# Optimization experiments

Hardware: AMD Instinct MI355X
Metric: run time of the kernel (lower is better)

## Reference

```python
import jax, jax.numpy as jnp
import numpy as np
from jax import lax

N = 50000        # num nodes
E = 800000       # edges per relation (no self loops; N self loops appended)
R = 3            # num_relations
F_IN = 256       # feature_size
C = 128          # hid_dim / channels
B = 4096         # batch_nodes
DT = 0.25
NSTEPS = 4       # n = ceil(time/dt) = ceil(1.0/0.25)


def setup_inputs() -> dict:
    key = jax.random.key(0)
    k1, k2, k3, k4, k5, k6, k7, k8 = jax.random.split(key, 8)
    features = jax.random.normal(k1, (N, F_IN), dtype=jnp.float32)
    # edges with no self loops: dst = (src + off) mod N, off in [1, N)
    src = jax.random.randint(k2, (R, E), 0, N)
    off = jax.random.randint(k3, (R, E), 1, N)
    dst = (src + off) % N
    edge_index = jnp.stack([src, dst], axis=1).astype(jnp.int64)  # [R, 2, E]
    batch_nodes = jax.random.randint(k4, (B,), 0, N).astype(jnp.int64)
    s = 1.0 / np.sqrt(F_IN)
    lin0_w = jax.random.normal(k5, (R, C, F_IN), dtype=jnp.float32) * s
    lin0_b = jax.random.normal(k6, (R, C), dtype=jnp.float32) * 0.01
    lin1_w = jax.random.normal(k7, (R, C, F_IN), dtype=jnp.float32) * s
    lin1_b = jax.random.normal(k8, (R, C), dtype=jnp.float32) * 0.01
    return {"features": features, "edge_index": edge_index, "batch_nodes": batch_nodes,
            "lin0_w": lin0_w, "lin0_b": lin0_b, "lin1_w": lin1_w, "lin1_b": lin1_b}


def _propagate(x, row, col, w):
    # out[i] = sum_{e: col[e]==i} w[e] * x[row[e]]   (gather-scale-scatter SpMM)
    return jax.ops.segment_sum(w[:, None] * x[row], col, num_segments=N)


def _wave_pde(x, row, col, w0, b0, w1, b1):
    # add_remaining_self_loops(fill=0.0): self loops appended at end with weight 0
    loops = jnp.arange(N, dtype=row.dtype)
    row_f = jnp.concatenate([row, loops])
    col_f = jnp.concatenate([col, loops])
    w_f = jnp.concatenate([jnp.ones((E,), x.dtype), jnp.zeros((N,), x.dtype)])
    # sym normalization: D^-1/2 A D^-1/2 (deg over col)
    deg = jax.ops.segment_sum(w_f, col_f, num_segments=N)
    dinv = jnp.where(deg > 0, lax.rsqrt(jnp.maximum(deg, 1e-30)), 0.0)
    w_norm = dinv[row_f] * w_f * dinv[col_f]
    # set_init_value
    phi0 = x @ w0.T + b0
    phi1 = x @ w1.T + b1
    # exp_conv_0 (exp_init=True): w' = dt^2*w/2; diag += 1; x1 = dt*phi1 + prop(phi0)
    w_init = (DT * DT * 0.5) * w_norm
    w_init = w_init.at[E:].add(1.0)
    x1 = DT * phi1 + _propagate(phi0, row_f, col_f, w_init)
    # time-stepping convs: w'' = dt^2*w; diag += 2; x_next = prop(x) - x_pre
    w_step = (DT * DT) * w_norm
    w_step = w_step.at[E:].add(2.0)

    def step(carry, _):
        xc, xp = carry
        xn = _propagate(xc, row_f, col_f, w_step) - xp
        return (xn, xc), None

    (x_out, _), _ = lax.scan(step, (x1, phi0), None, length=NSTEPS - 1)
    return x_out


def reference(features, edge_index, batch_nodes, lin0_w, lin0_b, lin1_w, lin1_b):
    # eval mode: dropout is identity
    embeds = []
    for r in range(R):
        row = edge_index[r, 0]
        col = edge_index[r, 1]
        x = _wave_pde(features, row, col, lin0_w[r], lin0_b[r], lin1_w[r], lin1_b[r])
        embeds.append(x[batch_nodes])  # [B, C]
    multi = jnp.stack(embeds, axis=1)  # [B, R, C]
    return multi.reshape(B, R * C)
```

## Files before the change

kernel.cpp:

```cpp
#include <hip/hip_runtime.h>
#include <hip/hip_bf16.h>

#define N_NODES 50000
#define N_EDGES 800000
#define N_REL   3
#define F_IN    256
#define CH      128
#define BATCH   4096
#define DT      0.25f

typedef __bf16 bf16x8 __attribute__((ext_vector_type(8)));
typedef float f32x4 __attribute__((ext_vector_type(4)));

__device__ __forceinline__ ushort f2bf(float f) {
  unsigned u = __float_as_uint(f);
  return (ushort)((u + 0x7FFFu + ((u >> 16) & 1u)) >> 16);
}
__device__ __forceinline__ float bf2f(ushort h) {
  return __uint_as_float((unsigned)h << 16);
}

__global__ void k_detect(const int* __restrict__ ei, int* __restrict__ flag) {
  int lane = threadIdx.x;
  int v = ei[2 * lane + 1];
  unsigned long long m = __ballot(v != 0);
  if (lane == 0) flag[0] = (m == 0ull) ? 1 : 0;
}

__global__ void k_hist3(const int* __restrict__ ei, const int* __restrict__ flag,
                        int* __restrict__ deg3) {
  int e = blockIdx.x * 256 + threadIdx.x;
  int r = blockIdx.y;
  if (e >= N_EDGES) return;
  long ci = (long)r * 2 * N_EDGES + N_EDGES + e;
  int d = flag[0] ? ei[2 * ci] : ei[ci];
  atomicAdd(&deg3[r * N_NODES + d], 1);
}

__global__ void k_dinv3(const int* __restrict__ deg3, float* __restrict__ dinv3) {
  int i = blockIdx.x * blockDim.x + threadIdx.x;
  if (i >= 3 * N_NODES) return;
  int d = deg3[i];
  dinv3[i] = d > 0 ? rsqrtf((float)d) : 0.0f;
}

__global__ void k_scan3(const int* __restrict__ deg3, int* __restrict__ off3) {
  __shared__ int sm[1024];
  const int* deg = deg3 + blockIdx.x * N_NODES;
  int* off = off3 + blockIdx.x * (N_NODES + 1);
  int tid = threadIdx.x;
  const int PER = (N_NODES + 1023) / 1024;
  int base = tid * PER;
  int s = 0;
  for (int i = 0; i < PER; ++i) { int idx = base + i; if (idx < N_NODES) s += deg[idx]; }
  sm[tid] = s;
  __syncthreads();
  for (int d = 1; d < 1024; d <<= 1) {
    int v = 0;
    if (tid >= d) v = sm[tid - d];
    __syncthreads();
    sm[tid] += v;
    __syncthreads();
  }
  int run = sm[tid] - s;
  for (int i = 0; i < PER; ++i) {
    int idx = base + i;
    if (idx < N_NODES) { off[idx] = run; run += deg[idx]; }
  }
  if (tid == 1023) off[N_NODES] = run;
}

__global__ void k_fill3(const int* __restrict__ ei, const int* __restrict__ flag,
                        const int* __restrict__ off3, int* __restrict__ cur3,
                        const float* __restrict__ dinv3, int2* __restrict__ csr) {
  int e = blockIdx.x * 256 + threadIdx.x;
  int r = blockIdx.y;
  if (e >= N_EDGES) return;
  int i64 = flag[0];
  long ri = (long)r * 2 * N_EDGES + e;
  long ci = ri + N_EDGES;
  int s = i64 ? ei[2 * ri] : ei[ri];
  int d = i64 ? ei[2 * ci] : ei[ci];
  const float* dinv = dinv3 + r * N_NODES;
  int pos = atomicAdd(&cur3[r * N_NODES + d], 1);
  int slot = off3[r * (N_NODES + 1) + d] + pos;
  csr[(size_t)r * N_EDGES + slot] = make_int2(s, __float_as_int(dinv[s] * dinv[d]));
}

__global__ __launch_bounds__(256) void k_phi_mfma(
    const float* __restrict__ X, const float* __restrict__ W0,
    const float* __restrict__ b0, const float* __restrict__ W1,
    const float* __restrict__ b1, float* __restrict__ P0,
    float* __restrict__ P1) {
  __shared__ ushort Ah[128 * 32], Al[128 * 32], Bh[128 * 32], Bl[128 * 32];
  const int tid = threadIdx.x;
  const int m0 = blockIdx.x * 128;
  const float* W = blockIdx.y ? W1 : W0;
  const float* bias = blockIdx.y ? b1 : b0;
  float* P = blockIdx.y ? P1 : P0;
  const int wid = tid >> 6, lane = tid & 63;
  const int wr = wid >> 1, wc = wid & 1;
  const int lr = lane & 15, k8 = lane >> 4;
  const int rt = tid >> 1, kb = (tid & 1) * 16;
  const bool mok = (m0 + rt) < N_NODES;
  const float* Xrow = X + (size_t)(m0 + rt) * F_IN;
  const float* Wrow = W + (size_t)rt * F_IN;
  f32x4 acc[4][4] = {};
  for (int k0 = 0; k0 < F_IN; k0 += 32) {
    float4 xa[4], wb[4];
#pragma unroll
    for (int j = 0; j < 4; ++j) {
      xa[j] = mok ? *(const float4*)(Xrow + k0 + kb + 4 * j)
                  : make_float4(0.f, 0.f, 0.f, 0.f);
      wb[j] = *(const float4*)(Wrow + k0 + kb + 4 * j);
    }
    if (k0) __syncthreads();
#pragma unroll
    for (int j = 0; j < 4; ++j) {
      int idx = rt * 32 + kb + 4 * j;
      ushort h0 = f2bf(xa[j].x), h1 = f2bf(xa[j].y), h2 = f2bf(xa[j].z), h3 = f2bf(xa[j].w);
      *(ushort4*)&Ah[idx] = make_ushort4(h0, h1, h2, h3);
      *(ushort4*)&Al[idx] =
          make_ushort4(f2bf(xa[j].x - bf2f(h0)), f2bf(xa[j].y - bf2f(h1)),
                       f2bf(xa[j].z - bf2f(h2)), f2bf(xa[j].w - bf2f(h3)));
      ushort g0 = f2bf(wb[j].x), g1 = f2bf(wb[j].y), g2 = f2bf(wb[j].z), g3 = f2bf(wb[j].w);
      *(ushort4*)&Bh[idx] = make_ushort4(g0, g1, g2, g3);
      *(ushort4*)&Bl[idx] =
          make_ushort4(f2bf(wb[j].x - bf2f(g0)), f2bf(wb[j].y - bf2f(g1)),
                       f2bf(wb[j].z - bf2f(g2)), f2bf(wb[j].w - bf2f(g3)));
    }
    __syncthreads();
    bf16x8 ah[4], al[4], bh[4], bl[4];
#pragma unroll
    for (int i = 0; i < 4; ++i) {
      int ao = (wr * 64 + i * 16 + lr) * 32 + k8 * 8;
      int bo = (wc * 64 + i * 16 + lr) * 32 + k8 * 8;
      ah[i] = *(const bf16x8*)&Ah[ao];
      al[i] = *(const bf16x8*)&Al[ao];
      bh[i] = *(const bf16x8*)&Bh[bo];
      bl[i] = *(const bf16x8*)&Bl[bo];
    }
#pragma unroll
    for (int i = 0; i < 4; ++i)
#pragma unroll
      for (int j = 0; j < 4; ++j) {
        acc[i][j] = __builtin_amdgcn_mfma_f32_16x16x32_bf16(ah[i], bh[j], acc[i][j], 0, 0, 0);
        acc[i][j] = __builtin_amdgcn_mfma_f32_16x16x32_bf16(ah[i], bl[j], acc[i][j], 0, 0, 0);
        acc[i][j] = __builtin_amdgcn_mfma_f32_16x16x32_bf16(al[i], bh[j], acc[i][j], 0, 0, 0);
      }
  }
#pragma unroll
  for (int j = 0; j < 4; ++j) {
    int ch = wc * 64 + j * 16 + lr;
    float bv = bias[ch];
#pragma unroll
    for (int i = 0; i < 4; ++i) {
      int mbase = m0 + wr * 64 + i * 16 + k8 * 4;
#pragma unroll
      for (int q = 0; q < 4; ++q) {
        int m = mbase + q;
        if (m < N_NODES) P[(size_t)m * CH + ch] = acc[i][j][q] + bv;
      }
    }
  }
}

__global__ __launch_bounds__(256, 6) void k_prop(
    const float* __restrict__ xc, const float* __restrict__ other,
    float* __restrict__ out, const int* __restrict__ off,
    const int2* __restrict__ csr, float wscale, float aself, float beta) {
  int node = blockIdx.x * 4 + (threadIdx.x >> 6);
  if (node >= N_NODES) return;
  int lane = threadIdx.x & 63;
  int g = lane >> 4, l = lane & 15;
  int e0 = off[node], e1 = off[node + 1];
  size_t base = (size_t)node * CH;
  int go = (g & 1) * 64;
  float4 sv = *(const float4*)(xc + base + go + 4 * l);
  float4 ov = *(const float4*)(other + base + go + 4 * l);
  float4 acc0 = make_float4(0.f, 0.f, 0.f, 0.f);
  float4 acc1 = make_float4(0.f, 0.f, 0.f, 0.f);
  for (int e = e0; e < e1; e += 16) {
    int lim = e1 - 1;
    int2 pm[4];
    float wgt[4];
#pragma unroll
    for (int u = 0; u < 4; ++u) {
      int ee = e + 4 * u + g;
      pm[u] = csr[min(ee, lim)];
      wgt[u] = (ee <= lim) ? __int_as_float(pm[u].y) : 0.f;
    }
    float4 va[4], vb[4];
#pragma unroll
    for (int u = 0; u < 4; ++u) {
      const float4* rs = (const float4*)(xc + (size_t)pm[u].x * CH);
      va[u] = rs[l];
      vb[u] = rs[l + 16];
    }
#pragma unroll
    for (int u = 0; u < 4; ++u) {
      float w0 = wgt[u];
      acc0.x = fmaf(w0, va[u].x, acc0.x); acc0.y = fmaf(w0, va[u].y, acc0.y);
      acc0.z = fmaf(w0, va[u].z, acc0.z); acc0.w = fmaf(w0, va[u].w, acc0.w);
      acc1.x = fmaf(w0, vb[u].x, acc1.x); acc1.y = fmaf(w0, vb[u].y, acc1.y);
      acc1.z = fmaf(w0, vb[u].z, acc1.z); acc1.w = fmaf(w0, vb[u].w, acc1.w);
    }
  }
#pragma unroll
  for (int m = 16; m < 64; m <<= 1) {
    acc0.x += __shfl_xor(acc0.x, m); acc0.y += __shfl_xor(acc0.y, m);
    acc0.z += __shfl_xor(acc0.z, m); acc0.w += __shfl_xor(acc0.w, m);
    acc1.x += __shfl_xor(acc1.x, m); acc1.y += __shfl_xor(acc1.y, m);
    acc1.z += __shfl_xor(acc1.z, m); acc1.w += __shfl_xor(acc1.w, m);
  }
  if (g == 0) {
    float4 o;
    o.x = wscale * acc0.x + aself * sv.x + beta * ov.x;
    o.y = wscale * acc0.y + aself * sv.y + beta * ov.y;
    o.z = wscale * acc0.z + aself * sv.z + beta * ov.z;
    o.w = wscale * acc0.w + aself * sv.w + beta * ov.w;
    *(float4*)(out + base + 4 * l) = o;
  } else if (g == 1) {
    float4 o;
    o.x = wscale * acc1.x + aself * sv.x + beta * ov.x;
    o.y = wscale * acc1.y + aself * sv.y + beta * ov.y;
    o.z = wscale * acc1.z + aself * sv.z + beta * ov.z;
    o.w = wscale * acc1.w + aself * sv.w + beta * ov.w;
    *(float4*)(out + base + 64 + 4 * l) = o;
  }
}

__global__ void k_gather(const float* __restrict__ x, const int* __restrict__ batch,
                         const int* __restrict__ flag, float* __restrict__ out, int r) {
  int idx = blockIdx.x * blockDim.x + threadIdx.x;
  int b = idx >> 6, lane = idx & 63;
  if (b >= BATCH) return;
  int i64 = flag[0];
  int node = i64 ? batch[2 * b] : batch[b];
  ((float2*)out)[(size_t)b * (N_REL * 64) + r * 64 + lane] =
      ((const float2*)x)[(size_t)node * 64 + lane];
}

extern "C" void kernel_launch(void* const* d_in, const int* in_sizes, int n_in,
                              void* d_out, int out_size, void* d_ws, size_t ws_size,
                              hipStream_t stream) {
  const float* features   = (const float*)d_in[0];
  const int*   edge_index = (const int*)d_in[1];
  const int*   batch_nodes= (const int*)d_in[2];
  const float* lin0_w     = (const float*)d_in[3];
  const float* lin0_b     = (const float*)d_in[4];
  const float* lin1_w     = (const float*)d_in[5];
  const float* lin1_b     = (const float*)d_in[6];
  float* out = (float*)d_out;

  char* w = (char*)d_ws;
  size_t o = 0;
  auto nxt = [&](size_t bytes) {
    char* p = w + o;
    o = (o + bytes + 255) & ~(size_t)255;
    return p;
  };
  int*   flag  = (int*)  nxt(256);
  int*   deg3  = (int*)  nxt((size_t)3 * N_NODES * 4);
  int*   cur3  = (int*)  nxt((size_t)3 * N_NODES * 4);
  float* dinv3 = (float*)nxt((size_t)3 * N_NODES * 4);
  int*   off3  = (int*)  nxt((size_t)3 * (N_NODES + 1) * 4);
  int2*  csr   = (int2*) nxt((size_t)3 * N_EDGES * 8);
  float* P0    = (float*)nxt((size_t)N_NODES * CH * 4);
  float* P1    = (float*)nxt((size_t)N_NODES * CH * 4);
  float* Ab    = (float*)nxt((size_t)N_NODES * CH * 4);

  k_detect<<<1, 64, 0, stream>>>(edge_index, flag);
  hipMemsetAsync(deg3, 0, (size_t)3 * N_NODES * 4, stream);
  hipMemsetAsync(cur3, 0, (size_t)3 * N_NODES * 4, stream);
  k_hist3<<<dim3((N_EDGES + 255) / 256, 3), 256, 0, stream>>>(edge_index, flag, deg3);
  k_dinv3<<<(3 * N_NODES + 255) / 256, 256, 0, stream>>>(deg3, dinv3);
  k_scan3<<<3, 1024, 0, stream>>>(deg3, off3);
  k_fill3<<<dim3((N_EDGES + 255) / 256, 3), 256, 0, stream>>>(edge_index, flag, off3,
                                                              cur3, dinv3, csr);

  const float h2 = DT * DT;
  for (int r = 0; r < N_REL; ++r) {
    const int*  offr = off3 + r * (N_NODES + 1);
    const int2* csrr = csr + (size_t)r * N_EDGES;
    k_phi_mfma<<<dim3((N_NODES + 127) / 128, 2), 256, 0, stream>>>(
        features, lin0_w + (size_t)r * CH * F_IN, lin0_b + (size_t)r * CH,
        lin1_w + (size_t)r * CH * F_IN, lin1_b + (size_t)r * CH, P0, P1);
    k_prop<<<(N_NODES + 3) / 4, 256, 0, stream>>>(P0, P1, Ab, offr, csrr,
                                                  0.5f * h2, 1.0f, DT);
    k_prop<<<(N_NODES + 3) / 4, 256, 0, stream>>>(Ab, P0, P0, offr, csrr,
                                                  h2, 2.0f, -1.0f);
    k_prop<<<(N_NODES + 3) / 4, 256, 0, stream>>>(P0, Ab, Ab, offr, csrr,
                                                  h2, 2.0f, -1.0f);
    k_prop<<<(N_NODES + 3) / 4, 256, 0, stream>>>(Ab, P0, P0, offr, csrr,
                                                  h2, 2.0f, -1.0f);
    k_gather<<<(BATCH * 64 + 255) / 256, 256, 0, stream>>>(P0, batch_nodes, flag, out, r);
  }
}
```

Measured before the change: 1.323 ms.

## Rescale features by D^-1/2, drop edge weights, fuse last propagation with batch gather

When every node has nonzero degree, the symmetric normalisation is folded into the features: phi outputs are pre-scaled by dinv, the CSR holds only source indices (halving edge traffic), and each propagation divides by the node degree, with a sqrt(deg) rescale at the output. A device flag set when any node has zero degree keeps the old weighted path as a fallback. The final time step is computed only for the batch nodes and written straight to the output, skipping one full-graph propagation per relation and the separate gather kernel. The change adds a branch on a runtime flag inside the hot loop and alters the floating-point rounding order.

```diff
diff --git a/kernel.cpp b/kernel.cpp
--- a/kernel.cpp
+++ b/kernel.cpp
@@ -37,11 +37,17 @@
   atomicAdd(&deg3[r * N_NODES + d], 1);
 }
 
-__global__ void k_dinv3(const int* __restrict__ deg3, float* __restrict__ dinv3) {
+__global__ void k_dinv3(const int* __restrict__ deg3, float* __restrict__ dinv3,
+                        int* __restrict__ flag) {
   int i = blockIdx.x * blockDim.x + threadIdx.x;
   if (i >= 3 * N_NODES) return;
   int d = deg3[i];
-  dinv3[i] = d > 0 ? rsqrtf((float)d) : 0.0f;
+  if (d > 0) {
+    dinv3[i] = rsqrtf((float)d);
+  } else {
+    dinv3[i] = 0.0f;
+    atomicOr(&flag[1], 1);
+  }
 }
 
 __global__ void k_scan3(const int* __restrict__ deg3, int* __restrict__ off3) {
@@ -72,25 +78,31 @@
 
 __global__ void k_fill3(const int* __restrict__ ei, const int* __restrict__ flag,
                         const int* __restrict__ off3, int* __restrict__ cur3,
-                        const float* __restrict__ dinv3, int2* __restrict__ csr) {
+                        const float* __restrict__ dinv3, void* __restrict__ csrv) {
   int e = blockIdx.x * 256 + threadIdx.x;
   int r = blockIdx.y;
   if (e >= N_EDGES) return;
-  int i64 = flag[0];
+  int i64 = flag[0], iso = flag[1];
   long ri = (long)r * 2 * N_EDGES + e;
   long ci = ri + N_EDGES;
   int s = i64 ? ei[2 * ri] : ei[ri];
   int d = i64 ? ei[2 * ci] : ei[ci];
-  const float* dinv = dinv3 + r * N_NODES;
   int pos = atomicAdd(&cur3[r * N_NODES + d], 1);
   int slot = off3[r * (N_NODES + 1) + d] + pos;
-  csr[(size_t)r * N_EDGES + slot] = make_int2(s, __float_as_int(dinv[s] * dinv[d]));
+  if (iso) {
+    const float* dinv = dinv3 + r * N_NODES;
+    ((int2*)csrv)[(size_t)r * N_EDGES + slot] =
+        make_int2(s, __float_as_int(dinv[s] * dinv[d]));
+  } else {
+    ((int*)csrv)[(size_t)r * N_EDGES + slot] = s;
+  }
 }
 
 __global__ __launch_bounds__(256) void k_phi_mfma(
     const float* __restrict__ X, const float* __restrict__ W0,
     const float* __restrict__ b0, const float* __restrict__ W1,
-    const float* __restrict__ b1, float* __restrict__ P0,
+    const float* __restrict__ b1, const float* __restrict__ dinv,
+    const int* __restrict__ flag, float* __restrict__ P0,
     float* __restrict__ P1) {
   __shared__ ushort Ah[128 * 32], Al[128 * 32], Bh[128 * 32], Bl[128 * 32];
   const int tid = threadIdx.x;
@@ -149,6 +161,15 @@
         acc[i][j] = __builtin_amdgcn_mfma_f32_16x16x32_bf16(al[i], bh[j], acc[i][j], 0, 0, 0);
       }
   }
+  int iso = flag[1];
+  float rsc[4][4];
+#pragma unroll
+  for (int i = 0; i < 4; ++i)
+#pragma unroll
+    for (int q = 0; q < 4; ++q) {
+      int m = m0 + wr * 64 + i * 16 + k8 * 4 + q;
+      rsc[i][q] = (m < N_NODES && !iso) ? dinv[m] : 1.0f;
+    }
 #pragma unroll
   for (int j = 0; j < 4; ++j) {
     int ch = wc * 64 + j * 16 + lr;
@@ -159,7 +180,67 @@
 #pragma unroll
       for (int q = 0; q < 4; ++q) {
         int m = mbase + q;
-        if (m < N_NODES) P[(size_t)m * CH + ch] = acc[i][j][q] + bv;
+        if (m < N_NODES) P[(size_t)m * CH + ch] = (acc[i][j][q] + bv) * rsc[i][q];
+      }
+    }
+  }
+}
+
+__device__ __forceinline__ void prop_accum(
+    const float* __restrict__ xc, const void* __restrict__ csrv, int r, int iso,
+    int e0, int e1, int g, int l, float4& acc0, float4& acc1) {
+  if (!iso) {
+    const int* csr = (const int*)csrv + (size_t)r * N_EDGES;
+    for (int e = e0; e < e1; e += 16) {
+      int lim = e1 - 1;
+      int src[4]; float wgt[4];
+#pragma unroll
+      for (int u = 0; u < 4; ++u) {
+        int ee = e + 4 * u + g;
+        src[u] = csr[min(ee, lim)];
+        wgt[u] = (ee <= lim) ? 1.f : 0.f;
+      }
+      float4 va[4], vb[4];
+#pragma unroll
+      for (int u = 0; u < 4; ++u) {
+        const float4* rs = (const float4*)(xc + (size_t)src[u] * CH);
+        va[u] = rs[l];
+        vb[u] = rs[l + 16];
+      }
+#pragma unroll
+      for (int u = 0; u < 4; ++u) {
+        float w0 = wgt[u];
+        acc0.x = fmaf(w0, va[u].x, acc0.x); acc0.y = fmaf(w0, va[u].y, acc0.y);
+        acc0.z = fmaf(w0, va[u].z, acc0.z); acc0.w = fmaf(w0, va[u].w, acc0.w);
+        acc1.x = fmaf(w0, vb[u].x, acc1.x); acc1.y = fmaf(w0, vb[u].y, acc1.y);
+        acc1.z = fmaf(w0, vb[u].z, acc1.z); acc1.w = fmaf(w0, vb[u].w, acc1.w);
+      }
+    }
+  } else {
+    const int2* csr = (const int2*)csrv + (size_t)r * N_EDGES;
+    for (int e = e0; e < e1; e += 16) {
+      int lim = e1 - 1;
+      int2 pm[4]; float wgt[4];
+#pragma unroll
+      for (int u = 0; u < 4; ++u) {
+        int ee = e + 4 * u + g;
+        pm[u] = csr[min(ee, lim)];
+        wgt[u] = (ee <= lim) ? __int_as_float(pm[u].y) : 0.f;
+      }
+      float4 va[4], vb[4];
+#pragma unroll
+      for (int u = 0; u < 4; ++u) {
+        const float4* rs = (const float4*)(xc + (size_t)pm[u].x * CH);
+        va[u] = rs[l];
+        vb[u] = rs[l + 16];
+      }
+#pragma unroll
+      for (int u = 0; u < 4; ++u) {
+        float w0 = wgt[u];
+        acc0.x = fmaf(w0, va[u].x, acc0.x); acc0.y = fmaf(w0, va[u].y, acc0.y);
+        acc0.z = fmaf(w0, va[u].z, acc0.z); acc0.w = fmaf(w0, va[u].w, acc0.w);
+        acc1.x = fmaf(w0, vb[u].x, acc1.x); acc1.y = fmaf(w0, vb[u].y, acc1.y);
+        acc1.z = fmaf(w0, vb[u].z, acc1.z); acc1.w = fmaf(w0, vb[u].w, acc1.w);
       }
     }
   }
@@ -168,9 +249,11 @@
 __global__ __launch_bounds__(256, 6) void k_prop(
     const float* __restrict__ xc, const float* __restrict__ other,
     float* __restrict__ out, const int* __restrict__ off,
-    const int2* __restrict__ csr, float wscale, float aself, float beta) {
+    const void* __restrict__ csrv, const int* __restrict__ flag, int r,
+    float wscale, float aself, float beta) {
   int node = blockIdx.x * 4 + (threadIdx.x >> 6);
   if (node >= N_NODES) return;
+  int iso = flag[1];
   int lane = threadIdx.x & 63;
   int g = lane >> 4, l = lane & 15;
   int e0 = off[node], e1 = off[node + 1];
@@ -180,32 +263,7 @@
   float4 ov = *(const float4*)(other + base + go + 4 * l);
   float4 acc0 = make_float4(0.f, 0.f, 0.f, 0.f);
   float4 acc1 = make_float4(0.f, 0.f, 0.f, 0.f);
-  for (int e = e0; e < e1; e += 16) {
-    int lim = e1 - 1;
-    int2 pm[4];
-    float wgt[4];
-#pragma unroll
-    for (int u = 0; u < 4; ++u) {
-      int ee = e + 4 * u + g;
-      pm[u] = csr[min(ee, lim)];
-      wgt[u] = (ee <= lim) ? __int_as_float(pm[u].y) : 0.f;
-    }
-    float4 va[4], vb[4];
-#pragma unroll
-    for (int u = 0; u < 4; ++u) {
-      const float4* rs = (const float4*)(xc + (size_t)pm[u].x * CH);
-      va[u] = rs[l];
-      vb[u] = rs[l + 16];
-    }
-#pragma unroll
-    for (int u = 0; u < 4; ++u) {
-      float w0 = wgt[u];
-      acc0.x = fmaf(w0, va[u].x, acc0.x); acc0.y = fmaf(w0, va[u].y, acc0.y);
-      acc0.z = fmaf(w0, va[u].z, acc0.z); acc0.w = fmaf(w0, va[u].w, acc0.w);
-      acc1.x = fmaf(w0, vb[u].x, acc1.x); acc1.y = fmaf(w0, vb[u].y, acc1.y);
-      acc1.z = fmaf(w0, vb[u].z, acc1.z); acc1.w = fmaf(w0, vb[u].w, acc1.w);
-    }
-  }
+  prop_accum(xc, csrv, r, iso, e0, e1, g, l, acc0, acc1);
 #pragma unroll
   for (int m = 16; m < 64; m <<= 1) {
     acc0.x += __shfl_xor(acc0.x, m); acc0.y += __shfl_xor(acc0.y, m);
@@ -213,32 +271,69 @@
     acc1.x += __shfl_xor(acc1.x, m); acc1.y += __shfl_xor(acc1.y, m);
     acc1.z += __shfl_xor(acc1.z, m); acc1.w += __shfl_xor(acc1.w, m);
   }
+  float ws2 = iso ? wscale : ((e1 > e0) ? wscale / (float)(e1 - e0) : 0.f);
   if (g == 0) {
     float4 o;
-    o.x = wscale * acc0.x + aself * sv.x + beta * ov.x;
-    o.y = wscale * acc0.y + aself * sv.y + beta * ov.y;
-    o.z = wscale * acc0.z + aself * sv.z + beta * ov.z;
-    o.w = wscale * acc0.w + aself * sv.w + beta * ov.w;
+    o.x = ws2 * acc0.x + aself * sv.x + beta * ov.x;
+    o.y = ws2 * acc0.y + aself * sv.y + beta * ov.y;
+    o.z = ws2 * acc0.z + aself * sv.z + beta * ov.z;
+    o.w = ws2 * acc0.w + aself * sv.w + beta * ov.w;
     *(float4*)(out + base + 4 * l) = o;
   } else if (g == 1) {
     float4 o;
-    o.x = wscale * acc1.x + aself * sv.x + beta * ov.x;
-    o.y = wscale * acc1.y + aself * sv.y + beta * ov.y;
-    o.z = wscale * acc1.z + aself * sv.z + beta * ov.z;
-    o.w = wscale * acc1.w + aself * sv.w + beta * ov.w;
+    o.x = ws2 * acc1.x + aself * sv.x + beta * ov.x;
+    o.y = ws2 * acc1.y + aself * sv.y + beta * ov.y;
+    o.z = ws2 * acc1.z + aself * sv.z + beta * ov.z;
+    o.w = ws2 * acc1.w + aself * sv.w + beta * ov.w;
     *(float4*)(out + base + 64 + 4 * l) = o;
   }
 }
 
-__global__ void k_gather(const float* __restrict__ x, const int* __restrict__ batch,
-                         const int* __restrict__ flag, float* __restrict__ out, int r) {
-  int idx = blockIdx.x * blockDim.x + threadIdx.x;
-  int b = idx >> 6, lane = idx & 63;
+__global__ __launch_bounds__(256) void k_gprop(
+    const float* __restrict__ y3, const float* __restrict__ y2,
+    const int* __restrict__ off, const void* __restrict__ csrv,
+    const int* __restrict__ flag, const int* __restrict__ batch,
+    float* __restrict__ out, int r, float wscale, float aself, float beta) {
+  int b = blockIdx.x * 4 + (threadIdx.x >> 6);
   if (b >= BATCH) return;
-  int i64 = flag[0];
+  int i64 = flag[0], iso = flag[1];
   int node = i64 ? batch[2 * b] : batch[b];
-  ((float2*)out)[(size_t)b * (N_REL * 64) + r * 64 + lane] =
-      ((const float2*)x)[(size_t)node * 64 + lane];
+  int lane = threadIdx.x & 63;
+  int g = lane >> 4, l = lane & 15;
+  int e0 = off[node], e1 = off[node + 1];
+  size_t base = (size_t)node * CH;
+  int go = (g & 1) * 64;
+  float4 sv = *(const float4*)(y3 + base + go + 4 * l);
+  float4 ov = *(const float4*)(y2 + base + go + 4 * l);
+  float4 acc0 = make_float4(0.f, 0.f, 0.f, 0.f);
+  float4 acc1 = make_float4(0.f, 0.f, 0.f, 0.f);
+  prop_accum(y3, csrv, r, iso, e0, e1, g, l, acc0, acc1);
+#pragma unroll
+  for (int m = 16; m < 64; m <<= 1) {
+    acc0.x += __shfl_xor(acc0.x, m); acc0.y += __shfl_xor(acc0.y, m);
+    acc0.z += __shfl_xor(acc0.z, m); acc0.w += __shfl_xor(acc0.w, m);
+    acc1.x += __shfl_xor(acc1.x, m); acc1.y += __shfl_xor(acc1.y, m);
+    acc1.z += __shfl_xor(acc1.z, m); acc1.w += __shfl_xor(acc1.w, m);
+  }
+  int deg = e1 - e0;
+  float ws2 = iso ? wscale : ((deg > 0) ? wscale / (float)deg : 0.f);
+  float osc = iso ? 1.0f : sqrtf((float)deg);
+  float* orow = out + (size_t)b * (N_REL * CH) + r * CH;
+  if (g == 0) {
+    float4 o;
+    o.x = osc * (ws2 * acc0.x + aself * sv.x + beta * ov.x);
+    o.y = osc * (ws2 * acc0.y + aself * sv.y + beta * ov.y);
+    o.z = osc * (ws2 * acc0.z + aself * sv.z + beta * ov.z);
+    o.w = osc * (ws2 * acc0.w + aself * sv.w + beta * ov.w);
+    *(float4*)(orow + 4 * l) = o;
+  } else if (g == 1) {
+    float4 o;
+    o.x = osc * (ws2 * acc1.x + aself * sv.x + beta * ov.x);
+    o.y = osc * (ws2 * acc1.y + aself * sv.y + beta * ov.y);
+    o.z = osc * (ws2 * acc1.z + aself * sv.z + beta * ov.z);
+    o.w = osc * (ws2 * acc1.w + aself * sv.w + beta * ov.w);
+    *(float4*)(orow + 64 + 4 * l) = o;
+  }
 }
 
 extern "C" void kernel_launch(void* const* d_in, const int* in_sizes, int n_in,
@@ -265,35 +360,36 @@
   int*   cur3  = (int*)  nxt((size_t)3 * N_NODES * 4);
   float* dinv3 = (float*)nxt((size_t)3 * N_NODES * 4);
   int*   off3  = (int*)  nxt((size_t)3 * (N_NODES + 1) * 4);
-  int2*  csr   = (int2*) nxt((size_t)3 * N_EDGES * 8);
+  void*  csr   = (void*) nxt((size_t)3 * N_EDGES * 8);
   float* P0    = (float*)nxt((size_t)N_NODES * CH * 4);
   float* P1    = (float*)nxt((size_t)N_NODES * CH * 4);
   float* Ab    = (float*)nxt((size_t)N_NODES * CH * 4);
 
-  k_detect<<<1, 64, 0, stream>>>(edge_index, flag);
+  hipMemsetAsync(flag, 0, 8, stream);
   hipMemsetAsync(deg3, 0, (size_t)3 * N_NODES * 4, stream);
   hipMemsetAsync(cur3, 0, (size_t)3 * N_NODES * 4, stream);
+  k_detect<<<1, 64, 0, stream>>>(edge_index, flag);
   k_hist3<<<dim3((N_EDGES + 255) / 256, 3), 256, 0, stream>>>(edge_index, flag, deg3);
-  k_dinv3<<<(3 * N_NODES + 255) / 256, 256, 0, stream>>>(deg3, dinv3);
+  k_dinv3<<<(3 * N_NODES + 255) / 256, 256, 0, stream>>>(deg3, dinv3, flag);
   k_scan3<<<3, 1024, 0, stream>>>(deg3, off3);
   k_fill3<<<dim3((N_EDGES + 255) / 256, 3), 256, 0, stream>>>(edge_index, flag, off3,
                                                               cur3, dinv3, csr);
 
   const float h2 = DT * DT;
   for (int r = 0; r < N_REL; ++r) {
-    const int*  offr = off3 + r * (N_NODES + 1);
-    const int2* csrr = csr + (size_t)r * N_EDGES;
+    const int* offr = off3 + r * (N_NODES + 1);
     k_phi_mfma<<<dim3((N_NODES + 127) / 128, 2), 256, 0, stream>>>(
         features, lin0_w + (size_t)r * CH * F_IN, lin0_b + (size_t)r * CH,
-        lin1_w + (size_t)r * CH * F_IN, lin1_b + (size_t)r * CH, P0, P1);
-    k_prop<<<(N_NODES + 3) / 4, 256, 0, stream>>>(P0, P1, Ab, offr, csrr,
+        lin1_w + (size_t)r * CH * F_IN, lin1_b + (size_t)r * CH,
+        dinv3 + r * N_NODES, flag, P0, P1);
+    k_prop<<<(N_NODES + 3) / 4, 256, 0, stream>>>(P0, P1, Ab, offr, csr, flag, r,
                                                   0.5f * h2, 1.0f, DT);
-    k_prop<<<(N_NODES + 3) / 4, 256, 0, stream>>>(Ab, P0, P0, offr, csrr,
+    k_prop<<<(N_NODES + 3) / 4, 256, 0, stream>>>(Ab, P0, P0, offr, csr, flag, r,
                                                   h2, 2.0f, -1.0f);
-    k_prop<<<(N_NODES + 3) / 4, 256, 0, stream>>>(P0, Ab, Ab, offr, csrr,
+    k_prop<<<(N_NODES + 3) / 4, 256, 0, stream>>>(P0, Ab, Ab, offr, csr, flag, r,
                                                   h2, 2.0f, -1.0f);
-    k_prop<<<(N_NODES + 3) / 4, 256, 0, stream>>>(Ab, P0, P0, offr, csrr,
-                                                  h2, 2.0f, -1.0f);
-    k_gather<<<(BATCH * 64 + 255) / 256, 256, 0, stream>>>(P0, batch_nodes, flag, out, r);
-  }
-}
+    k_gprop<<<(BATCH + 3) / 4, 256, 0, stream>>>(Ab, P0, offr, csr, flag,
+                                                 batch_nodes, out, r,
+                                                 h2, 2.0f, -1.0f);
+  }
+}
```

Measured after the change: 1.190 ms. 1.11x faster.
